# Kernel optimization log

Measured on AMD Instinct MI355X. Metric: run time of the kernel, lower is better.

The kernel has to match this reference:

```python
import jax, jax.numpy as jnp
import numpy as np

B = 16; SEQ_LEN = 96; PRED_LEN = 96; N_VARS = 862; D_MODEL = 512; D_FF = 1024
N_HEADS = 8; E_LAYERS = 2; D_FREQ = 512; KF_LEN = 5000; ALPHA = 0.5; TOP_P = 0.5
FREQ_DIM = SEQ_LEN // 2 + 1            # rfft bins = 49
KEY_LEN = int(np.ceil(FREQ_DIM * ALPHA))  # 25 -> y_freq in_features = 50
KERNEL = 25; NOISE_EPS = 0.01; LN_EPS = 1e-5; REVIN_EPS = 1e-5


def setup_inputs() -> dict:
    ks = iter(jax.random.split(jax.random.key(0), 64))
    def g(*shape):
        return jax.random.normal(next(ks), shape, jnp.float32) * 0.02
    z = lambda *s: jnp.zeros(s, jnp.float32)
    o = lambda *s: jnp.ones(s, jnp.float32)
    inp = {}
    inp['x_enc'] = jax.random.normal(next(ks), (B, SEQ_LEN, N_VARS), jnp.float32)
    inp['gate_noise'] = jax.random.normal(next(ks), (N_VARS,), jnp.float32)
    inp['revin_w'] = o(N_VARS); inp['revin_b'] = z(N_VARS)
    inp['fc2_w'] = g(SEQ_LEN, D_MODEL); inp['fc2_b'] = z(D_MODEL)
    inp['fc3_w'] = g(D_MODEL, PRED_LEN); inp['fc3_b'] = z(PRED_LEN)
    inp['fc4_w'] = g(SEQ_LEN, D_MODEL); inp['fc4_b'] = z(D_MODEL)
    inp['fc5_w'] = g(D_MODEL, PRED_LEN); inp['fc5_b'] = z(PRED_LEN)
    inp['tc_w1'] = g(D_MODEL, D_MODEL // 2); inp['tc_w2'] = g(D_MODEL // 2, N_VARS)
    inp['tn_w1'] = g(D_MODEL, D_MODEL // 2); inp['tn_w2'] = g(D_MODEL // 2, N_VARS)
    inp['lt_w1'] = g(SEQ_LEN, D_MODEL); inp['lt_b1'] = z(D_MODEL)
    inp['lt_w2'] = g(D_MODEL, D_MODEL); inp['lt_b2'] = z(D_MODEL)
    inp['yf_w'] = g(2 * KEY_LEN, D_FREQ); inp['yf_b'] = z(D_FREQ)
    inp['ls_w1'] = g(D_FREQ, D_FREQ); inp['ls_b1'] = z(D_FREQ)
    inp['ls_w2'] = g(D_FREQ, D_FREQ); inp['ls_b2'] = z(D_FREQ)
    inp['fco_w'] = g(2 * D_MODEL, PRED_LEN); inp['fco_b'] = z(PRED_LEN)
    inp['freq_table'] = jax.random.normal(next(ks), (KF_LEN, N_VARS), jnp.float32)
    inp['enc_wq'] = g(E_LAYERS, D_MODEL, D_MODEL); inp['enc_bq'] = z(E_LAYERS, D_MODEL)
    inp['enc_wk'] = g(E_LAYERS, D_MODEL, D_MODEL); inp['enc_bk'] = z(E_LAYERS, D_MODEL)
    inp['enc_wv'] = g(E_LAYERS, D_MODEL, D_MODEL); inp['enc_bv'] = z(E_LAYERS, D_MODEL)
    inp['enc_wo'] = g(E_LAYERS, D_MODEL, D_MODEL); inp['enc_bo'] = z(E_LAYERS, D_MODEL)
    inp['enc_c1w'] = g(E_LAYERS, D_MODEL, D_FF); inp['enc_c1b'] = z(E_LAYERS, D_FF)
    inp['enc_c2w'] = g(E_LAYERS, D_FF, D_MODEL); inp['enc_c2b'] = z(E_LAYERS, D_MODEL)
    inp['enc_g1'] = o(E_LAYERS, D_MODEL); inp['enc_be1'] = z(E_LAYERS, D_MODEL)
    inp['enc_g2'] = o(E_LAYERS, D_MODEL); inp['enc_be2'] = z(E_LAYERS, D_MODEL)
    inp['norm_g'] = o(D_MODEL); inp['norm_b'] = z(D_MODEL)
    inp['batch_key_frequency'] = jax.random.randint(next(ks), (B,), 0, KF_LEN)
    return inp


def _lrelu(t):
    return jnp.where(t >= 0, t, 0.01 * t)


def _layernorm(x, g, b):
    m = jnp.mean(x, -1, keepdims=True)
    v = jnp.mean((x - m) ** 2, -1, keepdims=True)
    return (x - m) * jax.lax.rsqrt(v + LN_EPS) * g + b


def _decomp(x):
    # moving_avg(kernel=25, stride=1) with edge replication padding, via cumsum
    pad = (KERNEL - 1) // 2
    xp = jnp.concatenate([jnp.repeat(x[:, :1], pad, axis=1), x,
                          jnp.repeat(x[:, -1:], pad, axis=1)], axis=1)
    c = jnp.cumsum(xp, axis=1)
    c = jnp.concatenate([jnp.zeros_like(c[:, :1]), c], axis=1)
    mean = (c[:, KERNEL:] - c[:, :-KERNEL]) / KERNEL  # [B, L, N]
    return x - mean, mean


def _kf_gather(table, index, length):
    # data[(index[:,None] + arange(length)) % KF_LEN] -> [B, length, N]
    gi = (index[:, None] + jnp.arange(length)[None, :]) % KF_LEN
    return table[gi]


def _forward(x_enc, gate_noise, revin_w, revin_b, fc2_w, fc2_b, fc3_w, fc3_b,
             fc4_w, fc4_b, fc5_w, fc5_b, tc_w1, tc_w2, tn_w1, tn_w2,
             lt_w1, lt_b1, lt_w2, lt_b2, yf_w, yf_b, ls_w1, ls_b1, ls_w2, ls_b2,
             fco_w, fco_b, freq_table, enc_wq, enc_bq, enc_wk, enc_bk, enc_wv, enc_bv,
             enc_wo, enc_bo, enc_c1w, enc_c1b, enc_c2w, enc_c2b,
             enc_g1, enc_be1, enc_g2, enc_be2, norm_g, norm_b, batch_key_frequency):
    # RevIN norm (stats detached, as in RevIN)
    mean = jax.lax.stop_gradient(jnp.mean(x_enc, axis=1, keepdims=True))
    std = jax.lax.stop_gradient(jnp.sqrt(jnp.var(x_enc, axis=1, keepdims=True) + REVIN_EPS))
    x = (x_enc - mean) / std * revin_w + revin_b  # [B, L, N]

    # ---- Frequency encoder ----
    _, trend = _decomp(x)
    t = _lrelu(trend.transpose(0, 2, 1) @ lt_w1 + lt_b1) @ lt_w2 + lt_b2  # [B,N,D]
    xf = jnp.fft.rfft(x.transpose(0, 2, 1), axis=-1, norm='ortho')  # [B,N,FREQ_DIM]
    y_key = jnp.concatenate([xf.real[..., :KEY_LEN], xf.imag[..., :KEY_LEN]], axis=-1)
    y_key = y_key @ yf_w + yf_b  # [B,N,D_FREQ]
    y_key = y_key.transpose(0, 2, 1) - _kf_gather(freq_table, batch_key_frequency, D_FREQ)
    y = _lrelu(y_key.transpose(0, 2, 1) @ ls_w1 + ls_b1) @ ls_w2 + ls_b2  # [B,N,D_FREQ]
    y = y.transpose(0, 2, 1) + _kf_gather(freq_table, (batch_key_frequency + D_FREQ) % KF_LEN, D_FREQ)
    y = y.transpose(0, 2, 1)  # [B,N,D_FREQ], real part of frequency coeffs
    x_fre = jnp.fft.irfft(y.astype(jnp.complex64), n=SEQ_LEN, axis=-1, norm='ortho')  # [B,N,L]
    x_fre = x_fre @ fc4_w + fc4_b + t  # [B,N,D]
    x_fre_loss = x_fre @ fc5_w + fc5_b  # [B,N,pred]

    # ---- Time encoder ----
    xb = x.transpose(0, 2, 1) @ fc2_w + fc2_b  # [B,N,D]
    # noisy top-p gating mask
    xc = jax.nn.relu(xb @ tc_w1) @ tc_w2
    xn = jax.nn.relu(xb @ tn_w1) @ tn_w2
    # nn.Softplus(beta=-1): -log(1+exp(-x)) = -softplus(-x)
    xe = xc + gate_noise * (-jax.nn.softplus(-(xn + NOISE_EPS)))
    xmin = jnp.min(xe, axis=-1, keepdims=True)
    xmax = jnp.max(xe, axis=-1, keepdims=True)
    logits = (xe - xmin) / (xmax - xmin + 1e-6) + jnp.eye(N_VARS, dtype=xe.dtype)
    mask = (logits < TOP_P)[:, None]  # [B,1,N,N], True = masked out

    scale = 1.0 / np.sqrt(D_MODEL // N_HEADS)
    for l in range(E_LAYERS):
        q = (xb @ enc_wq[l] + enc_bq[l]).reshape(B, N_VARS, N_HEADS, -1)
        k = (xb @ enc_wk[l] + enc_bk[l]).reshape(B, N_VARS, N_HEADS, -1)
        v = (xb @ enc_wv[l] + enc_bv[l]).reshape(B, N_VARS, N_HEADS, -1)
        s = jnp.einsum('blhe,bshe->bhls', q, k)
        s = jnp.where(mask, -jnp.inf, s)
        a = jax.nn.softmax(scale * s, axis=-1)
        o = jnp.einsum('bhls,bshd->blhd', a, v).reshape(B, N_VARS, D_MODEL)
        xb = xb + (o @ enc_wo[l] + enc_bo[l])
        xb = _layernorm(xb, enc_g1[l], enc_be1[l])
        yff = jax.nn.gelu(xb @ enc_c1w[l] + enc_c1b[l], approximate=False) @ enc_c2w[l] + enc_c2b[l]
        xb = _layernorm(xb + yff, enc_g2[l], enc_be2[l])
    xb = _layernorm(xb, norm_g, norm_b)
    x_time_loss = xb @ fc3_w + fc3_b  # [B,N,pred]

    dec = (jnp.concatenate([xb, x_fre], axis=-1) @ fco_w + fco_b).transpose(0, 2, 1)  # [B,pred,N]

    def _denorm(z):
        return ((z - revin_b) / (revin_w + REVIN_EPS * REVIN_EPS)) * std + mean

    dec = _denorm(dec)
    x_time_loss = _denorm(x_time_loss.transpose(0, 2, 1))
    x_fre_loss = _denorm(x_fre_loss.transpose(0, 2, 1))
    return dec[:, -PRED_LEN:, :], x_time_loss, x_fre_loss


def reference(x_enc, gate_noise, revin_w, revin_b, fc2_w, fc2_b, fc3_w, fc3_b,
              fc4_w, fc4_b, fc5_w, fc5_b, tc_w1, tc_w2, tn_w1, tn_w2,
              lt_w1, lt_b1, lt_w2, lt_b2, yf_w, yf_b, ls_w1, ls_b1, ls_w2, ls_b2,
              fco_w, fco_b, freq_table, enc_wq, enc_bq, enc_wk, enc_bk, enc_wv, enc_bv,
              enc_wo, enc_bo, enc_c1w, enc_c1b, enc_c2w, enc_c2b,
              enc_g1, enc_be1, enc_g2, enc_be2, norm_g, norm_b, batch_key_frequency):
    return _forward(x_enc, gate_noise, revin_w, revin_b, fc2_w, fc2_b, fc3_w, fc3_b,
                    fc4_w, fc4_b, fc5_w, fc5_b, tc_w1, tc_w2, tn_w1, tn_w2,
                    lt_w1, lt_b1, lt_w2, lt_b2, yf_w, yf_b, ls_w1, ls_b1, ls_w2, ls_b2,
                    fco_w, fco_b, freq_table, enc_wq, enc_bq, enc_wk, enc_bk, enc_wv, enc_bv,
                    enc_wo, enc_bo, enc_c1w, enc_c1b, enc_c2w, enc_c2b,
                    enc_g1, enc_be1, enc_g2, enc_be2, norm_g, norm_b, batch_key_frequency)
```

## Files before the change

### kernel.cpp

```cpp
#include <hip/hip_runtime.h>
#include <hip/hip_bf16.h>
#include <math.h>

typedef __hip_bfloat16 bf16;
typedef unsigned long long u64;
using s8v = __attribute__((ext_vector_type(8))) short;
using f4v = __attribute__((ext_vector_type(4))) float;

#define B_   16
#define L_   96
#define NV   862
#define DM   512
#define NH   8
#define DH   64
#define KFL  5000
#define NBN  (B_*NV)
#define NVP  896
#define QKVW 1536
#define L2P  128

#define BAR()  __builtin_amdgcn_s_barrier()
#define SCB()  __builtin_amdgcn_sched_barrier(0)
#define VMW0() asm volatile("s_waitcnt vmcnt(0)" ::: "memory")
#define VMW4() asm volatile("s_waitcnt vmcnt(4)" ::: "memory")
#define VMW6() asm volatile("s_waitcnt vmcnt(6)" ::: "memory")
#define VMW8() asm volatile("s_waitcnt vmcnt(8)" ::: "memory")

__device__ __forceinline__ float tof(bf16 x)  { return __bfloat162float(x); }

__device__ __forceinline__ int sxl(int r, int c) {
    return (r << 6) + ((c ^ (r & 7)) << 3);
}
__device__ __forceinline__ int px(int r, int k) {
    return (r << 6) + (((((k >> 3) ^ (r & 7)) + ((r & 8) >> 2)) & 7) << 3) + (k & 7);
}
__device__ __forceinline__ int pxc(int r, int c) {
    return (r << 6) + ((((c ^ (r & 7)) + ((r & 8) >> 2)) & 7) << 3);
}

__device__ __forceinline__ void gl16(const bf16* g, bf16* l)
{
    __builtin_amdgcn_global_load_lds(
        (const __attribute__((address_space(1))) void*)g,
        (__attribute__((address_space(3))) void*)l, 16, 0, 0);
}

__device__ __forceinline__ void stage64(const bf16* __restrict__ src, int ld,
                                        int r0, int rmax, int k0, bf16* buf, int tid)
{
    #pragma unroll
    for (int i = 0; i < 2; i++) {
        int e = tid + i * 256;
        int r = e >> 3, c = e & 7;
        int gr = r0 + r; gr = gr > rmax ? rmax : gr;
        int gk = k0 + ((c ^ (r & 7)) << 3);
        gl16(src + (size_t)gr * ld + gk, buf + ((size_t)(e >> 6) << 9));
    }
}
__device__ __forceinline__ void stage128(const bf16* __restrict__ src, int ld,
                                         int r0, int rmax, int k0, bf16* buf, int tid)
{
    #pragma unroll
    for (int i = 0; i < 4; i++) {
        int e = tid + i * 256;
        int r = e >> 3, c = e & 7;
        int gr = r0 + r; gr = gr > rmax ? rmax : gr;
        int gk = k0 + ((c ^ (r & 7)) << 3);
        gl16(src + (size_t)gr * ld + gk, buf + ((size_t)(e >> 6) << 9));
    }
}

__device__ __forceinline__ int xcd_swz(int orig, int nwg)
{
    int q = nwg >> 3, r = nwg & 7;
    int xc = orig & 7, loc = orig >> 3;
    return (xc < r ? xc * (q + 1) : r * (q + 1) + (xc - r) * q) + loc;
}

__global__ void detect_k(const unsigned short* __restrict__ rw, int* __restrict__ flag)
{
    if (threadIdx.x == 0 && blockIdx.x == 0)
        *flag = (rw[0] == 0 && rw[2] == 0 && rw[4] == 0) ? 1 : 0;
}

struct CB { const void* src[30]; bf16* dst[30]; int n[30]; int so[30]; };
__global__ __launch_bounds__(256)
void cvtb_k(CB cb, const int* __restrict__ flag)
{
    int t = blockIdx.y;
    int i = blockIdx.x * 256 + threadIdx.x;
    if (i >= cb.n[t]) return;
    int s = cb.so[t] + i;
    if (*flag) cb.dst[t][i] = __float2bfloat16(((const float*)cb.src[t])[s]);
    else       cb.dst[t][i] = ((const bf16*)cb.src[t])[s];
}

#define NWT 24
struct WD { const void* src; bf16* dst; int K, Kp, N; long srcOff; };
struct WTB { WD d[NWT]; };
__global__ __launch_bounds__(256)
void wtcb_k(WTB wb, const int* __restrict__ flag)
{
    __shared__ bf16 tile[32][33];
    WD dd = wb.d[blockIdx.z];
    int n0 = blockIdx.x * 32, k0 = blockIdx.y * 32;
    if (n0 >= dd.N || k0 >= dd.Kp) return;
    int tx = threadIdx.x & 31, ty = threadIdx.x >> 5;
    int f32 = *flag;
    #pragma unroll
    for (int r = 0; r < 4; r++) {
        int k = k0 + ty + r * 8, n = n0 + tx;
        bf16 v = __float2bfloat16(0.f);
        if (k < dd.K && n < dd.N)
            v = f32 ? __float2bfloat16(((const float*)dd.src)[dd.srcOff + (size_t)k * dd.N + n])
                    : ((const bf16*)dd.src)[dd.srcOff + (size_t)k * dd.N + n];
        tile[ty + r * 8][tx] = v;
    }
    __syncthreads();
    #pragma unroll
    for (int r = 0; r < 4; r++) {
        int n = n0 + ty + r * 8, k = k0 + tx;
        if (n < dd.N && k < dd.Kp) dd.dst[(size_t)n * dd.Kp + k] = tile[tx][ty + r * 8];
    }
}

__global__ __launch_bounds__(256)
void vt_k(const bf16* __restrict__ qkv, bf16* __restrict__ Vt)
{
    __shared__ bf16 t[32][33];
    int bh = blockIdx.z;
    int n0 = blockIdx.x * 32, d0 = blockIdx.y * 32;
    int b = bh >> 3, h = bh & 7;
    int tx = threadIdx.x & 31, ty = threadIdx.x >> 5;
    #pragma unroll
    for (int r = 0; r < 4; r++) {
        int n = n0 + ty + r * 8, d = d0 + tx;
        bf16 v = __float2bfloat16(0.f);
        if (n < NV) v = qkv[(size_t)(b * NV + n) * QKVW + 1024 + h * DH + d];
        t[ty + r * 8][tx] = v;
    }
    __syncthreads();
    #pragma unroll
    for (int r = 0; r < 4; r++) {
        int d = d0 + ty + r * 8, n = n0 + tx;
        Vt[((size_t)bh * DH + d) * NVP + n] = t[tx][ty + r * 8];
    }
}
// ... 40 lines not shown
        float xv = (v - m) / st * tof(rw[n]) + tof(rb[n]);
        xr[tid] = xv;
        xT[(size_t)row * L2P + tid] = __float2bfloat16(xv);
    } else {
        xT[(size_t)row * L2P + tid] = z16;
    }
    __syncthreads();
    if (tid < 96) {
        float acc = 0.f;
        #pragma unroll
        for (int d = -12; d <= 12; d++) {
            int k = tid + d;
            k = k < 0 ? 0 : (k > 95 ? 95 : k);
            acc += xr[k];
        }
        trend[(size_t)row * L2P + tid] = __float2bfloat16(acc * (1.f / 25.f));
    } else {
        trend[(size_t)row * L2P + tid] = z16;
    }
}

__global__ void myf_k(const bf16* __restrict__ yf_w, bf16* __restrict__ MyfT)
{
    int idx = blockIdx.x * 256 + threadIdx.x;
    if (idx >= 512 * L2P) return;
    int d = idx >> 7, l = idx & 127;
    const float invs = 0.10206207261596575f;
    float acc = 0.f;
    if (l < 96) {
        for (int f = 0; f < 25; f++) {
            float ang = (float)(f * l) / 48.0f;
            acc += cospif(ang) * tof(yf_w[f * 512 + d]);
            acc -= sinpif(ang) * tof(yf_w[(25 + f) * 512 + d]);
        }
        acc *= invs;
    }
    MyfT[(size_t)d * L2P + l] = __float2bfloat16(acc);
}

__global__ void ceff_k(const bf16* __restrict__ fc4_w, bf16* __restrict__ CeffT)
{
    int idx = blockIdx.x * 256 + threadIdx.x;
    if (idx >= 512 * 64) return;
    int d = idx >> 6, f = idx & 63;
    const float invs = 0.10206207261596575f;
    float acc = 0.f;
    if (f < 49) {
        for (int l = 0; l < 96; l++) {
            float coef;
            if (f == 0)       coef = 1.f;
            else if (f == 48) coef = (l & 1) ? -1.f : 1.f;
            else              coef = 2.f * cospif((float)(f * l) / 48.f);
            acc += coef * tof(fc4_w[l * 512 + d]);
        }
        acc *= invs;
    }
    CeffT[(size_t)d * 64 + f] = __float2bfloat16(acc);
}

__device__ __forceinline__ float epi(float v, int n, int m, int N, int act,
                                     const bf16* bias, const float* Res,
                                     const void* ft, const int* kf,
                                     const int* dflag)
{
    if (act >= 5) {
        v += tof(bias[n]);
        int b = m / NV, nv = m - b * NV;
        int gi = (act == 5) ? (kf[b] + n) % KFL : (kf[b] + 512 + n) % KFL;
        size_t gidx = (size_t)gi * NV + nv;
        float fv = (*dflag) ? ((const float*)ft)[gidx] : tof(((const bf16*)ft)[gidx]);
        return (act == 5) ? v - fv : v + fv;
    }
    if (act == 4) {
        float z = -(v + 0.01f);
        float sp = fmaxf(z, 0.f) + log1pf(expf(-fabsf(z)));
        return Res[(size_t)m * N + n] + tof(bias[n]) * (-sp);
    }
    if (bias) v += tof(bias[n]);
    if (Res)  v += Res[(size_t)m * N + n];
    if (act == 1)      v = fmaxf(v, 0.f);
    else if (act == 2) v = (v >= 0.f) ? v : 0.01f * v;
    else if (act == 3) v = 0.5f * v * (1.f + erff(v * 0.70710678118654752f));
    return v;
}

__global__ __launch_bounds__(256)
void gemm128c(const bf16* __restrict__ A, int lda,
              const bf16* __restrict__ Wt, int ldb,
              const bf16* __restrict__ bias, const float* Res,
              float* C32, bf16* C16, int M, int N, int K, int act, int gx)
{
    __shared__ __align__(16) bf16 As[2][128 * 64];
    __shared__ __align__(16) bf16 Bs[2][128 * 64];
    int tid = threadIdx.x;
    int w = tid >> 6, lane = tid & 63;
    int lr = lane >> 4, lc = lane & 15;
    int nid = xcd_swz(blockIdx.x, gridDim.x);
    int bx = nid % gx, by = nid / gx;
    int row0 = by * 128, col0 = bx * 128;
    int mq = (w >> 1) * 64, nq = (w & 1) * 64;
    f4v acc[4][4] = {};
    int nt = K >> 6;
    stage128(A, lda, row0, M - 1, 0, As[0], tid);
    stage128(Wt, ldb, col0, N - 1, 0, Bs[0], tid);
    if (nt > 1) {
        stage128(A, lda, row0, M - 1, 64, As[1], tid);
        stage128(Wt, ldb, col0, N - 1, 64, Bs[1], tid);
        VMW8();
    } else {
        VMW0();
    }
    BAR(); SCB();
    for (int t = 0; t < nt; t++) {
        int cur = t & 1;
        #pragma unroll
        for (int sub = 0; sub < 2; sub++) {
            int ck = sub * 4 + lr;
            s8v a[4], b[4];
            #pragma unroll
            for (int mt = 0; mt < 4; mt++) a[mt] = *(const s8v*)&As[cur][sxl(mq + mt * 16 + lc, ck)];
            #pragma unroll
            for (int j = 0; j < 4; j++) b[j] = *(const s8v*)&Bs[cur][sxl(nq + j * 16 + lc, ck)];
            #pragma unroll
            for (int mt = 0; mt < 4; mt++)
                #pragma unroll
                for (int j = 0; j < 4; j++)
                    acc[mt][j] = __builtin_amdgcn_mfma_f32_16x16x32_bf16(a[mt], b[j], acc[mt][j], 0, 0, 0);
        }
        if (t + 1 < nt) {
            SCB(); BAR(); SCB();
            if (t + 2 < nt) {
                stage128(A, lda, row0, M - 1, (t + 2) << 6, As[cur], tid);
                stage128(Wt, ldb, col0, N - 1, (t + 2) << 6, Bs[cur], tid);
                VMW8();
            } else {
                VMW0();
            }
            BAR(); SCB();
        }
    }
    #pragma unroll
    for (int mt = 0; mt < 4; mt++)
    #pragma unroll
    for (int j = 0; j < 4; j++) {
        #pragma unroll
        for (int r = 0; r < 4; r++) {
            int m = row0 + mq + mt * 16 + lr * 4 + r;
            int n = col0 + nq + j * 16 + lc;
            if (m >= M || n >= N) continue;
            float v = epi(acc[mt][j][r], n, m, N, act, bias, Res, nullptr, nullptr, nullptr);
            if (C32) C32[(size_t)m * N + n] = v;
            if (C16) C16[(size_t)m * N + n] = __float2bfloat16(v);
        }
    }
}

__global__ __launch_bounds__(256)
void gemm64c(const bf16* __restrict__ A, int lda,
             const bf16* __restrict__ Wt, int ldb,
             const bf16* __restrict__ bias, const float* Res,
             float* C32, bf16* C16, int M, int N, int K, int act,
             const void* ft, const int* kf, const int* dflag, int gx)
{
    __shared__ __align__(16) bf16 As[2][64 * 64];
    __shared__ __align__(16) bf16 Bs[2][128 * 64];
    int tid = threadIdx.x;
    int w = tid >> 6, lane = tid & 63;
    int lr = lane >> 4, lc = lane & 15;
    int nid = xcd_swz(blockIdx.x, gridDim.x);
    int bx = nid % gx, by = nid / gx;
    int row0 = by * 64, col0 = bx * 128;
    int mq = (w >> 1) * 32, nq = (w & 1) * 64;
    f4v acc[2][4] = {};
    int nt = K >> 6;
    stage64(A, lda, row0, M - 1, 0, As[0], tid);
    stage128(Wt, ldb, col0, N - 1, 0, Bs[0], tid);
    if (nt > 1) {
        stage64(A, lda, row0, M - 1, 64, As[1], tid);
        stage128(Wt, ldb, col0, N - 1, 64, Bs[1], tid);
        VMW6();
    } else {
        VMW0();
    }
    BAR(); SCB();
    for (int t = 0; t < nt; t++) {
        int cur = t & 1;
        #pragma unroll
        for (int sub = 0; sub < 2; sub++) {
            int ck = sub * 4 + lr;
            s8v a[2], b[4];
            #pragma unroll
            for (int mt = 0; mt < 2; mt++) a[mt] = *(const s8v*)&As[cur][sxl(mq + mt * 16 + lc, ck)];
            #pragma unroll
            for (int j = 0; j < 4; j++) b[j] = *(const s8v*)&Bs[cur][sxl(nq + j * 16 + lc, ck)];
            #pragma unroll
            for (int mt = 0; mt < 2; mt++)
                #pragma unroll
                for (int j = 0; j < 4; j++)
                    acc[mt][j] = __builtin_amdgcn_mfma_f32_16x16x32_bf16(a[mt], b[j], acc[mt][j], 0, 0, 0);
        }
        if (t + 1 < nt) {
            SCB(); BAR(); SCB();
            if (t + 2 < nt) {
                stage64(A, lda, row0, M - 1, (t + 2) << 6, As[cur], tid);
                stage128(Wt, ldb, col0, N - 1, (t + 2) << 6, Bs[cur], tid);
                VMW6();
            } else {
                VMW0();
            }
            BAR(); SCB();
        }
    }
    #pragma unroll
    for (int mt = 0; mt < 2; mt++)
    #pragma unroll
    for (int j = 0; j < 4; j++) {
        #pragma unroll
        for (int r = 0; r < 4; r++) {
            int m = row0 + mq + mt * 16 + lr * 4 + r;
            int n = col0 + nq + j * 16 + lc;
            if (m >= M || n >= N) continue;
            float v = epi(acc[mt][j][r], n, m, N, act, bias, Res, ft, kf, dflag);
            if (C32) C32[(size_t)m * N + n] = v;
            if (C16) C16[(size_t)m * N + n] = __float2bfloat16(v);
        }
    }
}

__global__ __launch_bounds__(256)
void outg_mfma(const bf16* __restrict__ xb16, const bf16* __restrict__ xfre16,
               const bf16* __restrict__ fcoT, const bf16* __restrict__ fc3T,
               const bf16* __restrict__ fc5T, const bf16* __restrict__ fcob,
               const bf16* __restrict__ fc3b, const bf16* __restrict__ fc5b,
               const bf16* __restrict__ rw, const bf16* __restrict__ rb,
               const float* __restrict__ meanA, const float* __restrict__ stdA,
               void* __restrict__ outv, const int* __restrict__ flag)
{
    __shared__ __align__(16) bf16 As[2][64 * 64];
    __shared__ __align__(16) bf16 Bs[2][64 * 64];
    const int M = NBN, N = 96;
    const size_t OSZ = (size_t)B_ * L_ * NV;
    int z = blockIdx.z;
    const bf16 *A1, *W1, *A2 = nullptr, *W2 = nullptr, *bias;
    int ldb; size_t obase;
    if (z == 0) { A1 = xb16; W1 = fcoT; A2 = xfre16; W2 = fcoT + 512; ldb = 1024; bias = fcob; obase = 0; }
    else if (z == 1) { A1 = xb16; W1 = fc3T; ldb = 512; bias = fc3b; obase = OSZ; }
    else { A1 = xfre16; W1 = fc5T; ldb = 512; bias = fc5b; obase = 2 * OSZ; }
    int tid = threadIdx.x;
    int w = tid >> 6, lane = tid & 63;
    int lr = lane >> 4, lc = lane & 15;
    int row0 = blockIdx.y * 64, col0 = blockIdx.x * 64;
    int mq = (w >> 1) * 32, nq = (w & 1) * 32;
    int f32o = *flag;
    f4v acc[2][2] = {};
    int nt = (z == 0) ? 16 : 8;
    stage64(A1, 512, row0, M - 1, 0, As[0], tid);
    stage64(W1, ldb, col0, N - 1, 0, Bs[0], tid);
    stage64(A1, 512, row0, M - 1, 64, As[1], tid);
    stage64(W1, ldb, col0, N - 1, 64, Bs[1], tid);
    VMW4();
    BAR(); SCB();
    for (int t = 0; t < nt; t++) {
        int cur = t & 1;
        #pragma unroll
        for (int sub = 0; sub < 2; sub++) {
            int ck = sub * 4 + lr;
            s8v a0 = *(const s8v*)&As[cur][sxl(mq + lc, ck)];
            s8v a1 = *(const s8v*)&As[cur][sxl(mq + 16 + lc, ck)];
            s8v b0 = *(const s8v*)&Bs[cur][sxl(nq + lc, ck)];
            s8v b1 = *(const s8v*)&Bs[cur][sxl(nq + 16 + lc, ck)];
            acc[0][0] = __builtin_amdgcn_mfma_f32_16x16x32_bf16(a0, b0, acc[0][0], 0, 0, 0);
            acc[0][1] = __builtin_amdgcn_mfma_f32_16x16x32_bf16(a0, b1, acc[0][1], 0, 0, 0);
            acc[1][0] = __builtin_amdgcn_mfma_f32_16x16x32_bf16(a1, b0, acc[1][0], 0, 0, 0);
            acc[1][1] = __builtin_amdgcn_mfma_f32_16x16x32_bf16(a1, b1, acc[1][1], 0, 0, 0);
        }
        if (t + 1 < nt) {
            SCB(); BAR(); SCB();
            if (t + 2 < nt) {
                int tn = t + 2;
                const bf16* Ax = (z == 0 && tn >= 8) ? A2 : A1;
                const bf16* Wx = (z == 0 && tn >= 8) ? W2 : W1;
                stage64(Ax, 512, row0, M - 1, (tn & 7) << 6, As[cur], tid);
                stage64(Wx, ldb, col0, N - 1, (tn & 7) << 6, Bs[cur], tid);
                VMW4();
            } else {
                VMW0();
            }
            BAR(); SCB();
        }
    }
    #pragma unroll
    for (int mt = 0; mt < 2; mt++)
    #pragma unroll
    for (int j = 0; j < 2; j++) {
        #pragma unroll
        for (int r = 0; r < 4; r++) {
            int m = row0 + mq + mt * 16 + lr * 4 + r;
            int c = col0 + nq + j * 16 + lc;
            if (m >= M || c >= N) continue;
            int b = m / NV, n = m - b * NV;
            float v = acc[mt][j][r] + tof(bias[c]);
            v = (v - tof(rb[n])) / (tof(rw[n]) + 1e-10f) * stdA[m] + meanA[m];
            size_t oidx = obase + ((size_t)b * L_ + c) * NV + n;
            if (f32o) ((float*)outv)[oidx] = v;
            else      ((bf16*)outv)[oidx] = __float2bfloat16(v);
        }
    }
// ... 166 lines not shown
    }

    const bf16* kbase = qkv + (size_t)b * NV * QKVW + 512 + hb;
    const bf16* vbase = Vt + (size_t)bh * DH * NVP;

    float lsum[4] = {0.f, 0.f, 0.f, 0.f};
    f4v oacc[4] = {};
    const int NT = 14;

    stage64(kbase, QKVW, 0, NV - 1, 0, Ks[0], tid);
    stage64(vbase, NVP, 0, DH - 1, 0, Vs[0], tid);
    stage64(kbase, QKVW, 64, NV - 1, 0, Ks[1], tid);
    stage64(vbase, NVP, 0, DH - 1, 64, Vs[1], tid);
    VMW4();
    BAR(); SCB();

    for (int t = 0; t < NT; t++) {
        int cur = t & 1;
        f4v s[4];
        __builtin_amdgcn_s_setprio(1);
        #pragma unroll
        for (int nt = 0; nt < 4; nt++) {
            f4v sacc = {0.f, 0.f, 0.f, 0.f};
            #pragma unroll
            for (int sub = 0; sub < 2; sub++) {
                s8v bb = *(const s8v*)&Ks[cur][sxl(nt * 16 + lc, sub * 4 + lr)];
                sacc = __builtin_amdgcn_mfma_f32_16x16x32_bf16(qf[sub], bb, sacc, 0, 0, 0);
            }
            s[nt] = sacc;
        }
        __builtin_amdgcn_s_setprio(0);
        #pragma unroll
        for (int r = 0; r < 4; r++) {
            int gq = qw + lr * 4 + r;
            u64 wd = (gq < NV) ? mask64[(size_t)(b * NV + gq) * 16 + t] : ~0ull;
            #pragma unroll
            for (int nt = 0; nt < 4; nt++) {
                float p = ((wd >> (nt * 16 + lc)) & 1) ? 0.f : exp2f(s[nt][r] * C);
                Pt[w][px(lr * 4 + r, nt * 16 + lc)] = __float2bfloat16(p);
                lsum[r] += p;
            }
        }
        #pragma unroll
        for (int sub = 0; sub < 2; sub++) {
            s8v pa = *(const s8v*)&Pt[w][pxc(lc, sub * 4 + lr)];
            __builtin_amdgcn_s_setprio(1);
            #pragma unroll
            for (int dt = 0; dt < 4; dt++) {
                s8v vv = *(const s8v*)&Vs[cur][sxl(dt * 16 + lc, sub * 4 + lr)];
                oacc[dt] = __builtin_amdgcn_mfma_f32_16x16x32_bf16(pa, vv, oacc[dt], 0, 0, 0);
            }
            __builtin_amdgcn_s_setprio(0);
        }
        if (t + 1 < NT) {
            SCB(); BAR(); SCB();
            if (t + 2 < NT) {
                int j2 = (t + 2) * 64;
                stage64(kbase, QKVW, j2, NV - 1, 0, Ks[cur], tid);
                stage64(vbase, NVP, 0, DH - 1, j2, Vs[cur], tid);
                VMW4();
            } else {
                VMW0();
            }
            BAR(); SCB();
        }
    }
    #pragma unroll
    for (int r = 0; r < 4; r++) {
        #pragma unroll
        for (int o2 = 1; o2 < 16; o2 <<= 1) lsum[r] += __shfl_xor(lsum[r], o2, 64);
    }
    #pragma unroll
    for (int r = 0; r < 4; r++) {
        int gq = qw + lr * 4 + r;
        if (gq >= NV) continue;
        float linv = 1.f / fmaxf(lsum[r], 1e-30f);
        #pragma unroll
        for (int dt = 0; dt < 4; dt++)
            O[((size_t)(b * NV + gq)) * DM + hb + dt * 16 + lc] =
                __float2bfloat16(oacc[dt][r] * linv);
    }
}

static void G1(hipStream_t s, const bf16* A, int lda, const bf16* Wt, int ldb,
               const bf16* bias, const float* Res, float* C32, bf16* C16,
               int M, int N, int K, int act)
{
    int gx = (N + 127) / 128, gy = (M + 127) / 128;
    gemm128c<<<dim3(gx * gy), 256, 0, s>>>(A, lda, Wt, ldb, bias, Res, C32, C16, M, N, K, act, gx);
}
static void G64(hipStream_t s, const bf16* A, int lda, const bf16* Wt, int ldb,
                const bf16* bias, const float* Res, float* C32, bf16* C16,
                int M, int N, int K, int act,
                const void* ft = nullptr, const int* kf = nullptr, const int* df = nullptr)
{
    int gx = (N + 127) / 128, gy = (M + 63) / 64;
    gemm64c<<<dim3(gx * gy), 256, 0, s>>>(A, lda, Wt, ldb, bias, Res, C32, C16, M, N, K, act, ft, kf, df, gx);
}

enum { I_XENC = 0, I_GNOISE, I_RW, I_RB, I_FC2W, I_FC2B, I_FC3W, I_FC3B,
       I_FC4W, I_FC4B, I_FC5W, I_FC5B, I_TCW1, I_TCW2, I_TNW1, I_TNW2,
       I_LTW1, I_LTB1, I_LTW2, I_LTB2, I_YFW, I_YFB, I_LSW1, I_LSB1,
       I_LSW2, I_LSB2, I_FCOW, I_FCOB, I_FT, I_EWQ, I_EBQ, I_EWK, I_EBK,
       I_EWV, I_EBV, I_EWO, I_EBO, I_C1W, I_C1B, I_C2W, I_C2B,
       I_G1, I_BE1, I_G2, I_BE2, I_NG, I_NB };

extern "C" void kernel_launch(void* const* d_in, const int* in_sizes, int n_in,
                              void* d_out, int out_size, void* d_ws, size_t ws_size,
                              hipStream_t stream)
{
    const int* bkey = (const int*)d_in[47];
    (void)ws_size; (void)in_sizes; (void)n_in; (void)out_size;

    float* ws = (float*)d_ws;
    size_t off = 0;
    auto alloc = [&](size_t nf) { nf = (nf + 3) & ~(size_t)3; float* p = ws + off; off += nf; return p; };
    auto balloc = [&](size_t nb) { return (bf16*)alloc((nb + 1) / 2); };
    int*  flag  = (int*)alloc(16);
    bf16* gnoise = balloc(862); bf16* rw = balloc(862); bf16* rb = balloc(862);
    bf16* fc2b = balloc(512);  bf16* fc3b = balloc(96);
    bf16* fc4w_c = balloc(49152); bf16* fc4b = balloc(512); bf16* fc5b = balloc(96);
    bf16* ltb1 = balloc(512);  bf16* ltb2 = balloc(512);
    bf16* yfw_c = balloc(25600); bf16* yfb = balloc(512);
    bf16* lsb1 = balloc(512);  bf16* lsb2 = balloc(512);
    bf16* fcob = balloc(96);
    bf16* qkvb = balloc(2 * QKVW);
    bf16* ebo = balloc(1024);  bf16* c1b = balloc(2048); bf16* c2b = balloc(1024);
    bf16* g1v = balloc(1024);  bf16* be1v = balloc(1024);
    bf16* g2v = balloc(1024);  bf16* be2v = balloc(1024);
    bf16* ngv = balloc(512);   bf16* nbv = balloc(512);
    bf16* fc2wT = balloc(512 * L2P);  bf16* fc3wT = balloc(49152); bf16* fc5wT = balloc(49152);
    bf16* lt1T = balloc(512 * L2P);   bf16* lt2T = balloc(262144);
    bf16* ls1T = balloc(262144);  bf16* ls2T = balloc(262144);
    bf16* fcoT = balloc(98304);
    bf16* tc2T = balloc(220672);  bf16* tn2T = balloc(220672);
    bf16* gate1w = balloc(262144);
    bf16* qkvw = balloc(2 * QKVW * 512);
    bf16* woT = balloc(524288);
    bf16* c1T = balloc(1048576);  bf16* c2T = balloc(1048576);
    bf16* xT    = balloc((size_t)NBN * L2P);
    bf16* trend = balloc((size_t)NBN * L2P);
    float* meanA = alloc(13824);
    float* stdA  = alloc(13824);
    bf16* MyfT  = balloc(512 * L2P);
    bf16* CeffT = balloc(512 * 64);
    bf16* y49   = balloc((size_t)NBN * 64);
    float* xb32 = alloc((size_t)NBN * 512);
    bf16* xb16  = balloc((size_t)NBN * 512);
    bf16* xfre16 = balloc((size_t)NBN * 512);
    bf16* tmp16 = balloc((size_t)NBN * 1024);
    float* fbuf = alloc((size_t)NBN * 512);
    float* gbuf = alloc((size_t)NBN * 1024);
    u64* mask64 = (u64*)alloc((size_t)NBN * 32);

    float* xe = gbuf;
    bf16* yA  = (bf16*)gbuf;
    bf16* qkv16 = (bf16*)gbuf;
    bf16* O16 = qkv16 + (size_t)NBN * QKVW;
    bf16* Vt  = tmp16;

    detect_k<<<1, 64, 0, stream>>>((const unsigned short*)d_in[I_RW], flag);

    {
        CB cb;
        int k = 0;
        auto add = [&](int idx, bf16* dst, int n, int so) {
            cb.src[k] = d_in[idx]; cb.dst[k] = dst; cb.n[k] = n; cb.so[k] = so; k++;
        };
        add(I_GNOISE, gnoise, 862, 0); add(I_RW, rw, 862, 0); add(I_RB, rb, 862, 0);
        add(I_FC2B, fc2b, 512, 0); add(I_FC3B, fc3b, 96, 0);
        add(I_FC4W, fc4w_c, 49152, 0); add(I_FC4B, fc4b, 512, 0); add(I_FC5B, fc5b, 96, 0);
        add(I_LTB1, ltb1, 512, 0); add(I_LTB2, ltb2, 512, 0);
        add(I_YFW, yfw_c, 25600, 0); add(I_YFB, yfb, 512, 0);
        add(I_LSB1, lsb1, 512, 0); add(I_LSB2, lsb2, 512, 0);
        add(I_FCOB, fcob, 96, 0);
        add(I_EBQ, qkvb + 0, 512, 0);          add(I_EBQ, qkvb + QKVW, 512, 512);
        add(I_EBK, qkvb + 512, 512, 0);        add(I_EBK, qkvb + QKVW + 512, 512, 512);
        add(I_EBV, qkvb + 1024, 512, 0);       add(I_EBV, qkvb + QKVW + 1024, 512, 512);
        add(I_EBO, ebo, 1024, 0); add(I_C1B, c1b, 2048, 0); add(I_C2B, c2b, 1024, 0);
        add(I_G1, g1v, 1024, 0); add(I_BE1, be1v, 1024, 0);
        add(I_G2, g2v, 1024, 0); add(I_BE2, be2v, 1024, 0);
        add(I_NG, ngv, 512, 0); add(I_NB, nbv, 512, 0);
        cvtb_k<<<dim3(192, 30), 256, 0, stream>>>(cb, flag);
    }

    {
        WTB wb;
        int k = 0;
        auto add = [&](int idx, bf16* dst, int K, int Kp, int N, long soff) {
            wb.d[k].src = d_in[idx]; wb.d[k].dst = dst;
            wb.d[k].K = K; wb.d[k].Kp = Kp; wb.d[k].N = N; wb.d[k].srcOff = soff; k++;
        };
        add(I_FC2W, fc2wT, 96, L2P, 512, 0);
        add(I_FC3W, fc3wT, 512, 512, 96, 0);
        add(I_FC5W, fc5wT, 512, 512, 96, 0);
        add(I_LTW1, lt1T, 96, L2P, 512, 0);
        add(I_LTW2, lt2T, 512, 512, 512, 0);
        add(I_LSW1, ls1T, 512, 512, 512, 0);
        add(I_LSW2, ls2T, 512, 512, 512, 0);
        add(I_FCOW, fcoT, 1024, 1024, 96, 0);
        add(I_TCW2, tc2T, 256, 256, 862, 0);
        add(I_TNW2, tn2T, 256, 256, 862, 0);
        add(I_TCW1, gate1w, 512, 512, 256, 0);
        add(I_TNW1, gate1w + 256 * 512, 512, 512, 256, 0);
        for (int l = 0; l < 2; l++) {
            add(I_EWO, woT + (size_t)l * 262144, 512, 512, 512, (long)l * 262144);
            add(I_C1W, c1T + (size_t)l * 524288, 512, 512, 1024, (long)l * 524288);
            add(I_C2W, c2T + (size_t)l * 524288, 1024, 1024, 512, (long)l * 524288);
            add(I_EWQ, qkvw + (size_t)l * 786432 + 0,      512, 512, 512, (long)l * 262144);
            add(I_EWK, qkvw + (size_t)l * 786432 + 262144, 512, 512, 512, (long)l * 262144);
            add(I_EWV, qkvw + (size_t)l * 786432 + 524288, 512, 512, 512, (long)l * 262144);
        }
        wtcb_k<<<dim3(32, 32, NWT), 256, 0, stream>>>(wb, flag);
    }

    revin_k<<<NBN, 128, 0, stream>>>(d_in[I_XENC], rw, rb, xT, trend, meanA, stdA, flag);
    myf_k<<<(512 * L2P + 255) / 256, 256, 0, stream>>>(yfw_c, MyfT);
    ceff_k<<<(512 * 64 + 255) / 256, 256, 0, stream>>>(fc4w_c, CeffT);

    G64(stream, trend, L2P, lt1T, L2P, ltb1, nullptr, nullptr, tmp16, NBN, 512, L2P, 2);
    G64(stream, tmp16, 512, lt2T, 512, ltb2, nullptr, fbuf, nullptr, NBN, 512, 512, 0);
    G64(stream, xT, L2P, MyfT, L2P, yfb, nullptr, nullptr, yA, NBN, 512, L2P, 5,
        d_in[I_FT], bkey, flag);
    G64(stream, yA, 512, ls1T, 512, lsb1, nullptr, nullptr, tmp16, NBN, 512, 512, 2);
    G64(stream, tmp16, 512, ls2T, 512, lsb2, nullptr, nullptr, y49, NBN, 64, 512, 6,
        d_in[I_FT], bkey, flag);
    G64(stream, y49, 64, CeffT, 64, fc4b, fbuf, nullptr, xfre16, NBN, 512, 64, 0);

    G64(stream, xT, L2P, fc2wT, L2P, fc2b, nullptr, xb32, xb16, NBN, 512, L2P, 0);

    G64(stream, xb16, 512, gate1w, 512, nullptr, nullptr, nullptr, tmp16, NBN, 512, 512, 1);
    G64(stream, tmp16, 512, tc2T, 256, nullptr, nullptr, xe, nullptr, NBN, 862, 256, 0);
    G64(stream, tmp16 + 256, 512, tn2T, 256, gnoise, xe, xe, nullptr, NBN, 862, 256, 4);
    gating_k<<<NBN, 256, 0, stream>>>(xe, mask64);

    for (int l = 0; l < 2; l++) {
        G1(stream, xb16, 512, qkvw + (size_t)l * QKVW * 512, 512,
           qkvb + l * QKVW, nullptr, nullptr, qkv16, NBN, QKVW, 512, 0);
        vt_k<<<dim3(NVP / 32, DH / 32, B_ * NH), 256, 0, stream>>>(qkv16, Vt);
        attn_k<<<dim3(14 * 128), 256, 0, stream>>>(qkv16, Vt, mask64, O16);
        G64(stream, O16, 512, woT + (size_t)l * 262144, 512, ebo + l * 512,
            xb32, fbuf, nullptr, NBN, 512, 512, 0);
        ln_k<<<NBN, 256, 0, stream>>>(fbuf, g1v + l * 512, be1v + l * 512, xb32, xb16);
        G1(stream, xb16, 512, c1T + (size_t)l * 524288, 512, c1b + l * 1024,
           nullptr, nullptr, tmp16, NBN, 1024, 512, 3);
        G64(stream, tmp16, 1024, c2T + (size_t)l * 524288, 1024, c2b + l * 512,
            xb32, fbuf, nullptr, NBN, 512, 1024, 0);
        if (l == 0)
            ln_k<<<NBN, 256, 0, stream>>>(fbuf, g2v, be2v, xb32, xb16);
        else
            ln2x_k<<<NBN, 256, 0, stream>>>(fbuf, g2v + 512, be2v + 512, ngv, nbv, xb16);
    }

    outg_mfma<<<dim3(2, (NBN + 63) / 64, 3), 256, 0, stream>>>(
        xb16, xfre16, fcoT, fc3wT, fc5wT, fcob, fc3b, fc5b,
        rw, rb, meanA, stdA, d_out, flag);
}
```

Baseline: 1.563 ms.

## Make GEMM kernels persistent with a pipeline that prefetches across tiles

```diff
diff --git a/kernel.cpp b/kernel.cpp
--- a/kernel.cpp
+++ b/kernel.cpp
@@ -275,31 +275,37 @@
 void gemm128c(const bf16* __restrict__ A, int lda,
               const bf16* __restrict__ Wt, int ldb,
               const bf16* __restrict__ bias, const float* Res,
-              float* C32, bf16* C16, int M, int N, int K, int act, int gx)
+              float* C32, bf16* C16, int M, int N, int K, int act,
+              int gx, int ntile)
 {
     __shared__ __align__(16) bf16 As[2][128 * 64];
     __shared__ __align__(16) bf16 Bs[2][128 * 64];
     int tid = threadIdx.x;
     int w = tid >> 6, lane = tid & 63;
     int lr = lane >> 4, lc = lane & 15;
-    int nid = xcd_swz(blockIdx.x, gridDim.x);
-    int bx = nid % gx, by = nid / gx;
-    int row0 = by * 128, col0 = bx * 128;
+    int nblk = gridDim.x;
+    int sb = xcd_swz(blockIdx.x, nblk);
     int mq = (w >> 1) * 64, nq = (w & 1) * 64;
+    int ntk = K >> 6;
+    int nmine = (ntile - 1 - sb) / nblk + 1;
+    int S = nmine * ntk;
     f4v acc[4][4] = {};
-    int nt = K >> 6;
-    stage128(A, lda, row0, M - 1, 0, As[0], tid);
-    stage128(Wt, ldb, col0, N - 1, 0, Bs[0], tid);
-    if (nt > 1) {
-        stage128(A, lda, row0, M - 1, 64, As[1], tid);
-        stage128(Wt, ldb, col0, N - 1, 64, Bs[1], tid);
-        VMW8();
-    } else {
-        VMW0();
-    }
+    const f4v z4 = {0.f, 0.f, 0.f, 0.f};
+
+    auto SSTEP = [&](int s, int buf) {
+        int tt = (s / ntk) * nblk + sb;
+        int bx = tt % gx, by = tt / gx;
+        int k0 = (s % ntk) << 6;
+        stage128(A, lda, by * 128, M - 1, k0, As[buf], tid);
+        stage128(Wt, ldb, bx * 128, N - 1, k0, Bs[buf], tid);
+    };
+
+    SSTEP(0, 0);
+    if (S > 1) { SSTEP(1, 1); VMW8(); } else { VMW0(); }
     BAR(); SCB();
-    for (int t = 0; t < nt; t++) {
-        int cur = t & 1;
+
+    for (int s = 0; s < S; s++) {
+        int cur = s & 1;
         #pragma unroll
         for (int sub = 0; sub < 2; sub++) {
             int ck = sub * 4 + lr;
@@ -314,30 +320,38 @@
                 for (int j = 0; j < 4; j++)
                     acc[mt][j] = __builtin_amdgcn_mfma_f32_16x16x32_bf16(a[mt], b[j], acc[mt][j], 0, 0, 0);
         }
-        if (t + 1 < nt) {
+        if (s + 1 < S) {
             SCB(); BAR(); SCB();
-            if (t + 2 < nt) {
-                stage128(A, lda, row0, M - 1, (t + 2) << 6, As[cur], tid);
-                stage128(Wt, ldb, col0, N - 1, (t + 2) << 6, Bs[cur], tid);
+            if (s + 2 < S) {
+                SSTEP(s + 2, cur);
                 VMW8();
             } else {
                 VMW0();
             }
             BAR(); SCB();
         }
-    }
-    #pragma unroll
-    for (int mt = 0; mt < 4; mt++)
-    #pragma unroll
-    for (int j = 0; j < 4; j++) {
-        #pragma unroll
-        for (int r = 0; r < 4; r++) {
-            int m = row0 + mq + mt * 16 + lr * 4 + r;
-            int n = col0 + nq + j * 16 + lc;
-            if (m >= M || n >= N) continue;
-            float v = epi(acc[mt][j][r], n, m, N, act, bias, Res, nullptr, nullptr, nullptr);
-            if (C32) C32[(size_t)m * N + n] = v;
-            if (C16) C16[(size_t)m * N + n] = __float2bfloat16(v);
+        if ((s % ntk) == ntk - 1) {
+            int tt = (s / ntk) * nblk + sb;
+            int bx = tt % gx, by = tt / gx;
+            int row0 = by * 128, col0 = bx * 128;
+            #pragma unroll
+            for (int mt = 0; mt < 4; mt++)
+            #pragma unroll
+            for (int j = 0; j < 4; j++) {
+                #pragma unroll
+                for (int r = 0; r < 4; r++) {
+                    int m = row0 + mq + mt * 16 + lr * 4 + r;
+                    int n = col0 + nq + j * 16 + lc;
+                    if (m >= M || n >= N) continue;
+                    float v = epi(acc[mt][j][r], n, m, N, act, bias, Res, nullptr, nullptr, nullptr);
+                    if (C32) C32[(size_t)m * N + n] = v;
+                    if (C16) C16[(size_t)m * N + n] = __float2bfloat16(v);
+                }
+            }
+            #pragma unroll
+            for (int mt = 0; mt < 4; mt++)
+                #pragma unroll
+                for (int j = 0; j < 4; j++) acc[mt][j] = z4;
         }
     }
 }
@@ -347,31 +361,37 @@
              const bf16* __restrict__ Wt, int ldb,
              const bf16* __restrict__ bias, const float* Res,
              float* C32, bf16* C16, int M, int N, int K, int act,
-             const void* ft, const int* kf, const int* dflag, int gx)
+             const void* ft, const int* kf, const int* dflag,
+             int gx, int ntile)
 {
     __shared__ __align__(16) bf16 As[2][64 * 64];
     __shared__ __align__(16) bf16 Bs[2][128 * 64];
     int tid = threadIdx.x;
     int w = tid >> 6, lane = tid & 63;
     int lr = lane >> 4, lc = lane & 15;
-    int nid = xcd_swz(blockIdx.x, gridDim.x);
-    int bx = nid % gx, by = nid / gx;
-    int row0 = by * 64, col0 = bx * 128;
+    int nblk = gridDim.x;
+    int sb = xcd_swz(blockIdx.x, nblk);
     int mq = (w >> 1) * 32, nq = (w & 1) * 64;
+    int ntk = K >> 6;
+    int nmine = (ntile - 1 - sb) / nblk + 1;
+    int S = nmine * ntk;
     f4v acc[2][4] = {};
-    int nt = K >> 6;
-    stage64(A, lda, row0, M - 1, 0, As[0], tid);
-    stage128(Wt, ldb, col0, N - 1, 0, Bs[0], tid);
-    if (nt > 1) {
-        stage64(A, lda, row0, M - 1, 64, As[1], tid);
-        stage128(Wt, ldb, col0, N - 1, 64, Bs[1], tid);
-        VMW6();
-    } else {
-        VMW0();
-    }
+    const f4v z4 = {0.f, 0.f, 0.f, 0.f};
+
+    auto SSTEP = [&](int s, int buf) {
+        int tt = (s / ntk) * nblk + sb;
+        int bx = tt % gx, by = tt / gx;
+        int k0 = (s % ntk) << 6;
+        stage64(A, lda, by * 64, M - 1, k0, As[buf], tid);
+        stage128(Wt, ldb, bx * 128, N - 1, k0, Bs[buf], tid);
+    };
+
+    SSTEP(0, 0);
+    if (S > 1) { SSTEP(1, 1); VMW6(); } else { VMW0(); }
     BAR(); SCB();
-    for (int t = 0; t < nt; t++) {
-        int cur = t & 1;
+
+    for (int s = 0; s < S; s++) {
+        int cur = s & 1;
         #pragma unroll
         for (int sub = 0; sub < 2; sub++) {
             int ck = sub * 4 + lr;
@@ -386,30 +406,38 @@
                 for (int j = 0; j < 4; j++)
                     acc[mt][j] = __builtin_amdgcn_mfma_f32_16x16x32_bf16(a[mt], b[j], acc[mt][j], 0, 0, 0);
         }
-        if (t + 1 < nt) {
+        if (s + 1 < S) {
             SCB(); BAR(); SCB();
-            if (t + 2 < nt) {
-                stage64(A, lda, row0, M - 1, (t + 2) << 6, As[cur], tid);
-                stage128(Wt, ldb, col0, N - 1, (t + 2) << 6, Bs[cur], tid);
+            if (s + 2 < S) {
+                SSTEP(s + 2, cur);
                 VMW6();
             } else {
                 VMW0();
             }
             BAR(); SCB();
         }
-    }
-    #pragma unroll
-    for (int mt = 0; mt < 2; mt++)
-    #pragma unroll
-    for (int j = 0; j < 4; j++) {
-        #pragma unroll
-        for (int r = 0; r < 4; r++) {
-            int m = row0 + mq + mt * 16 + lr * 4 + r;
-            int n = col0 + nq + j * 16 + lc;
-            if (m >= M || n >= N) continue;
-            float v = epi(acc[mt][j][r], n, m, N, act, bias, Res, ft, kf, dflag);
-            if (C32) C32[(size_t)m * N + n] = v;
-            if (C16) C16[(size_t)m * N + n] = __float2bfloat16(v);
+        if ((s % ntk) == ntk - 1) {
+            int tt = (s / ntk) * nblk + sb;
+            int bx = tt % gx, by = tt / gx;
+            int row0 = by * 64, col0 = bx * 128;
+            #pragma unroll
+            for (int mt = 0; mt < 2; mt++)
+            #pragma unroll
+            for (int j = 0; j < 4; j++) {
+                #pragma unroll
+                for (int r = 0; r < 4; r++) {
+                    int m = row0 + mq + mt * 16 + lr * 4 + r;
+                    int n = col0 + nq + j * 16 + lc;
+                    if (m >= M || n >= N) continue;
+                    float v = epi(acc[mt][j][r], n, m, N, act, bias, Res, ft, kf, dflag);
+                    if (C32) C32[(size_t)m * N + n] = v;
+                    if (C16) C16[(size_t)m * N + n] = __float2bfloat16(v);
+                }
+            }
+            #pragma unroll
+            for (int mt = 0; mt < 2; mt++)
+                #pragma unroll
+                for (int j = 0; j < 4; j++) acc[mt][j] = z4;
         }
     }
 }
@@ -747,7 +775,10 @@
                int M, int N, int K, int act)
 {
     int gx = (N + 127) / 128, gy = (M + 127) / 128;
-    gemm128c<<<dim3(gx * gy), 256, 0, s>>>(A, lda, Wt, ldb, bias, Res, C32, C16, M, N, K, act, gx);
+    int ntile = gx * gy;
+    int nblk = ntile < 512 ? ntile : 512;
+    gemm128c<<<dim3(nblk), 256, 0, s>>>(A, lda, Wt, ldb, bias, Res, C32, C16,
+                                        M, N, K, act, gx, ntile);
 }
 static void G64(hipStream_t s, const bf16* A, int lda, const bf16* Wt, int ldb,
                 const bf16* bias, const float* Res, float* C32, bf16* C16,
@@ -755,7 +786,10 @@
                 const void* ft = nullptr, const int* kf = nullptr, const int* df = nullptr)
 {
     int gx = (N + 127) / 128, gy = (M + 63) / 64;
-    gemm64c<<<dim3(gx * gy), 256, 0, s>>>(A, lda, Wt, ldb, bias, Res, C32, C16, M, N, K, act, ft, kf, df, gx);
+    int ntile = gx * gy;
+    int nblk = ntile < 768 ? ntile : 768;
+    gemm64c<<<dim3(nblk), 256, 0, s>>>(A, lda, Wt, ldb, bias, Res, C32, C16,
+                                       M, N, K, act, ft, kf, df, gx, ntile);
 }
 
 enum { I_XENC = 0, I_GNOISE, I_RW, I_RB, I_FC2W, I_FC2B, I_FC3W, I_FC3B,
```

Result: slower. 1.612 ms (+3.1%).

## Add 256x256-tile 512-thread GEMM kernel and route transformer and MLP GEMMs to it

Applied to the files above, without the earlier changes.

```diff
diff --git a/kernel.cpp b/kernel.cpp
--- a/kernel.cpp
+++ b/kernel.cpp
@@ -63,6 +63,18 @@
     #pragma unroll
     for (int i = 0; i < 4; i++) {
         int e = tid + i * 256;
+        int r = e >> 3, c = e & 7;
+        int gr = r0 + r; gr = gr > rmax ? rmax : gr;
+        int gk = k0 + ((c ^ (r & 7)) << 3);
+        gl16(src + (size_t)gr * ld + gk, buf + ((size_t)(e >> 6) << 9));
+    }
+}
+__device__ __forceinline__ void stage256w(const bf16* __restrict__ src, int ld,
+                                          int r0, int rmax, int k0, bf16* buf, int tid)
+{
+    #pragma unroll
+    for (int i = 0; i < 4; i++) {
+        int e = tid + i * 512;
         int r = e >> 3, c = e & 7;
         int gr = r0 + r; gr = gr > rmax ? rmax : gr;
         int gk = k0 + ((c ^ (r & 7)) << 3);
@@ -269,6 +281,84 @@
     else if (act == 2) v = (v >= 0.f) ? v : 0.01f * v;
     else if (act == 3) v = 0.5f * v * (1.f + erff(v * 0.70710678118654752f));
     return v;
+}
+
+__global__ __launch_bounds__(512)
+void gemm256(const bf16* __restrict__ A, int lda,
+             const bf16* __restrict__ Wt, int ldb,
+             const bf16* __restrict__ bias, const float* Res,
+             float* C32, bf16* C16, int M, int N, int K, int act, int gx)
+{
+    __shared__ __align__(16) bf16 As[2][256 * 64];
+    __shared__ __align__(16) bf16 Bs[2][256 * 64];
+    int tid = threadIdx.x;
+    int w = tid >> 6, lane = tid & 63;
+    int lr = lane >> 4, lc = lane & 15;
+    int nid = xcd_swz(blockIdx.x, gridDim.x);
+    int bx = nid % gx, by = nid / gx;
+    int row0 = by * 256, col0 = bx * 256;
+    int mq = (w >> 1) * 64;
+    int nq = (w & 1) * 128;
+    f4v acc[4][8] = {};
+    int nt = K >> 6;
+    stage256w(A, lda, row0, M - 1, 0, As[0], tid);
+    stage256w(Wt, ldb, col0, N - 1, 0, Bs[0], tid);
+    if (nt > 1) {
+        stage256w(A, lda, row0, M - 1, 64, As[1], tid);
+        stage256w(Wt, ldb, col0, N - 1, 64, Bs[1], tid);
+        VMW8();
+    } else {
+        VMW0();
+    }
+    BAR(); SCB();
+    for (int t = 0; t < nt; t++) {
+        int cur = t & 1;
+        #pragma unroll
+        for (int sub = 0; sub < 2; sub++) {
+            int ck = sub * 4 + lr;
+            s8v a[4];
+            #pragma unroll
+            for (int mt = 0; mt < 4; mt++) a[mt] = *(const s8v*)&As[cur][sxl(mq + mt * 16 + lc, ck)];
+            #pragma unroll
+            for (int jh = 0; jh < 2; jh++) {
+                s8v b[4];
+                #pragma unroll
+                for (int j = 0; j < 4; j++)
+                    b[j] = *(const s8v*)&Bs[cur][sxl(nq + jh * 64 + j * 16 + lc, ck)];
+                #pragma unroll
+                for (int mt = 0; mt < 4; mt++)
+                    #pragma unroll
+                    for (int j = 0; j < 4; j++)
+                        acc[mt][jh * 4 + j] = __builtin_amdgcn_mfma_f32_16x16x32_bf16(
+                            a[mt], b[j], acc[mt][jh * 4 + j], 0, 0, 0);
+            }
+        }
+        if (t + 1 < nt) {
+            SCB(); BAR(); SCB();
+            if (t + 2 < nt) {
+                stage256w(A, lda, row0, M - 1, (t + 2) << 6, As[cur], tid);
+                stage256w(Wt, ldb, col0, N - 1, (t + 2) << 6, Bs[cur], tid);
+                VMW8();
+            } else {
+                VMW0();
+            }
+            BAR(); SCB();
+        }
+    }
+    #pragma unroll
+    for (int mt = 0; mt < 4; mt++)
+    #pragma unroll
+    for (int j = 0; j < 8; j++) {
+        #pragma unroll
+        for (int r = 0; r < 4; r++) {
+            int m = row0 + mq + mt * 16 + lr * 4 + r;
+            int n = col0 + nq + j * 16 + lc;
+            if (m >= M || n >= N) continue;
+            float v = epi(acc[mt][j][r], n, m, N, act, bias, Res, nullptr, nullptr, nullptr);
+            if (C32) C32[(size_t)m * N + n] = v;
+            if (C16) C16[(size_t)m * N + n] = __float2bfloat16(v);
+        }
+    }
 }
 
 __global__ __launch_bounds__(256)
@@ -742,6 +832,14 @@
     }
 }
 
+static void G256(hipStream_t s, const bf16* A, int lda, const bf16* Wt, int ldb,
+                 const bf16* bias, const float* Res, float* C32, bf16* C16,
+                 int M, int N, int K, int act)
+{
+    int gx = (N + 255) / 256, gy = (M + 255) / 256;
+    gemm256<<<dim3(gx * gy), 512, 0, s>>>(A, lda, Wt, ldb, bias, Res, C32, C16,
+                                          M, N, K, act, gx);
+}
 static void G1(hipStream_t s, const bf16* A, int lda, const bf16* Wt, int ldb,
                const bf16* bias, const float* Res, float* C32, bf16* C16,
                int M, int N, int K, int act)
@@ -879,33 +977,33 @@
     ceff_k<<<(512 * 64 + 255) / 256, 256, 0, stream>>>(fc4w_c, CeffT);
 
     G64(stream, trend, L2P, lt1T, L2P, ltb1, nullptr, nullptr, tmp16, NBN, 512, L2P, 2);
-    G64(stream, tmp16, 512, lt2T, 512, ltb2, nullptr, fbuf, nullptr, NBN, 512, 512, 0);
+    G256(stream, tmp16, 512, lt2T, 512, ltb2, nullptr, fbuf, nullptr, NBN, 512, 512, 0);
     G64(stream, xT, L2P, MyfT, L2P, yfb, nullptr, nullptr, yA, NBN, 512, L2P, 5,
         d_in[I_FT], bkey, flag);
-    G64(stream, yA, 512, ls1T, 512, lsb1, nullptr, nullptr, tmp16, NBN, 512, 512, 2);
+    G256(stream, yA, 512, ls1T, 512, lsb1, nullptr, nullptr, tmp16, NBN, 512, 512, 2);
     G64(stream, tmp16, 512, ls2T, 512, lsb2, nullptr, nullptr, y49, NBN, 64, 512, 6,
         d_in[I_FT], bkey, flag);
     G64(stream, y49, 64, CeffT, 64, fc4b, fbuf, nullptr, xfre16, NBN, 512, 64, 0);
 
     G64(stream, xT, L2P, fc2wT, L2P, fc2b, nullptr, xb32, xb16, NBN, 512, L2P, 0);
 
-    G64(stream, xb16, 512, gate1w, 512, nullptr, nullptr, nullptr, tmp16, NBN, 512, 512, 1);
+    G256(stream, xb16, 512, gate1w, 512, nullptr, nullptr, nullptr, tmp16, NBN, 512, 512, 1);
     G64(stream, tmp16, 512, tc2T, 256, nullptr, nullptr, xe, nullptr, NBN, 862, 256, 0);
     G64(stream, tmp16 + 256, 512, tn2T, 256, gnoise, xe, xe, nullptr, NBN, 862, 256, 4);
     gating_k<<<NBN, 256, 0, stream>>>(xe, mask64);
 
     for (int l = 0; l < 2; l++) {
-        G1(stream, xb16, 512, qkvw + (size_t)l * QKVW * 512, 512,
-           qkvb + l * QKVW, nullptr, nullptr, qkv16, NBN, QKVW, 512, 0);
+        G256(stream, xb16, 512, qkvw + (size_t)l * QKVW * 512, 512,
+             qkvb + l * QKVW, nullptr, nullptr, qkv16, NBN, QKVW, 512, 0);
         vt_k<<<dim3(NVP / 32, DH / 32, B_ * NH), 256, 0, stream>>>(qkv16, Vt);
         attn_k<<<dim3(14 * 128), 256, 0, stream>>>(qkv16, Vt, mask64, O16);
-        G64(stream, O16, 512, woT + (size_t)l * 262144, 512, ebo + l * 512,
-            xb32, fbuf, nullptr, NBN, 512, 512, 0);
+        G256(stream, O16, 512, woT + (size_t)l * 262144, 512, ebo + l * 512,
+             xb32, fbuf, nullptr, NBN, 512, 512, 0);
         ln_k<<<NBN, 256, 0, stream>>>(fbuf, g1v + l * 512, be1v + l * 512, xb32, xb16);
-        G1(stream, xb16, 512, c1T + (size_t)l * 524288, 512, c1b + l * 1024,
-           nullptr, nullptr, tmp16, NBN, 1024, 512, 3);
-        G64(stream, tmp16, 1024, c2T + (size_t)l * 524288, 1024, c2b + l * 512,
-            xb32, fbuf, nullptr, NBN, 512, 1024, 0);
+        G256(stream, xb16, 512, c1T + (size_t)l * 524288, 512, c1b + l * 1024,
+             nullptr, nullptr, tmp16, NBN, 1024, 512, 3);
+        G256(stream, tmp16, 1024, c2T + (size_t)l * 524288, 1024, c2b + l * 512,
+             xb32, fbuf, nullptr, NBN, 512, 1024, 0);
         if (l == 0)
             ln_k<<<NBN, 256, 0, stream>>>(fbuf, g2v, be2v, xb32, xb16);
         else
```

After: 2.492 ms. +59.5%, slower.
